# Kernel optimization log

Measured on AMD Instinct MI355X. Metric: run time of the kernel, lower is better.

The kernel has to match this reference:

```python
import jax, jax.numpy as jnp
import numpy as np

N = 50000   # nodes
E = 600000  # edges
D = 128     # node_features (EvolveGCNO in=out channels)
H = 128     # hidden_dim (final Linear out)


def setup_inputs() -> dict:
    key = jax.random.key(0)
    ks = jax.random.split(key, 9)
    stdv = 1.0 / np.sqrt(D)
    u = lambda k, shape: jax.random.uniform(k, shape, jnp.float32, -stdv, stdv)
    return {
        "x": jax.random.normal(ks[0], (N, D), jnp.float32),
        "edge_index": jax.random.randint(ks[1], (2, E), 0, N),
        "edge_weight": jax.random.uniform(ks[2], (E,), jnp.float32),
        "W0": u(ks[3], (D, D)),        # EvolveGCNO initial_weight (squeezed)
        "w_ih": u(ks[4], (3 * D, D)),  # GRU input weights (r|z|n)
        "w_hh": u(ks[5], (3 * D, D)),  # GRU hidden weights (r|z|n)
        "b_ih": u(ks[6], (3 * D,)),
        "b_hh": u(ks[7], (3 * D,)),
        "W_lin": u(ks[8], (H, D)),     # torch Linear weight [out, in]
        "b_lin": jnp.zeros((H,), jnp.float32),
    }


def _gru_step(x, h, w_ih, w_hh, b_ih, b_hh):
    # One torch.nn.GRU cell step; here x == h == W0 (weight evolution).
    gi = x @ w_ih.T + b_ih
    gh = h @ w_hh.T + b_hh
    i_r, i_z, i_n = jnp.split(gi, 3, axis=-1)
    h_r, h_z, h_n = jnp.split(gh, 3, axis=-1)
    r = jax.nn.sigmoid(i_r + h_r)
    z = jax.nn.sigmoid(i_z + h_z)
    n = jnp.tanh(i_n + r * h_n)
    return (1.0 - z) * n + z * h


def reference(x, edge_index, edge_weight, W0, w_ih, w_hh, b_ih, b_hh, W_lin, b_lin):
    # 1) Evolve the GCN weight with one GRU step (input = hidden = W0).
    W = _gru_step(W0, W0, w_ih, w_hh, b_ih, b_hh)  # [D, D]

    # 2) GCNConv_Fixed_W: add self-loops (weight 1), symmetric normalization.
    loops = jnp.arange(N)
    row = jnp.concatenate([edge_index[0], loops])  # source
    col = jnp.concatenate([edge_index[1], loops])  # target
    ew = jnp.concatenate([edge_weight, jnp.ones((N,), x.dtype)])
    deg = jax.ops.segment_sum(ew, col, num_segments=N)
    dinv = jnp.where(deg > 0, jax.lax.rsqrt(deg), 0.0)
    norm = dinv[row] * ew * dinv[col]  # [E+N]

    xw = x @ W                                        # [N, D]
    h = jax.ops.segment_sum(norm[:, None] * xw[row], col, num_segments=N)  # [N, D]

    # 3) ReLU + Linear
    h = jax.nn.relu(h)
    return h @ W_lin.T + b_lin  # [N, H]
```

## Files before the change

kernel.cpp:

```cpp
#include <hip/hip_runtime.h>
#include <hip/hip_bf16.h>

#define NN 50000
#define EE 600000
#define DD 128
#define CAP 48

typedef __attribute__((ext_vector_type(8))) __bf16 bf16x8;
typedef __attribute__((ext_vector_type(8))) short short8;
typedef __attribute__((ext_vector_type(4))) float f32x4;

__device__ __forceinline__ unsigned short f2bf(float f) {
    union { float f; unsigned u; } c; c.f = f;
    unsigned r = (c.u + 0x7fffu + ((c.u >> 16) & 1u)) >> 16;
    return (unsigned short)r;
}
__device__ __forceinline__ float bflo(unsigned u) {
    union { unsigned u; float f; } c; c.u = u << 16; return c.f;
}
__device__ __forceinline__ float bfhi(unsigned u) {
    union { unsigned u; float f; } c; c.u = u & 0xffff0000u; return c.f;
}

__global__ __launch_bounds__(256) void gru_kernel(
    const float* __restrict__ W0, const float* __restrict__ w_ih,
    const float* __restrict__ w_hh, const float* __restrict__ b_ih,
    const float* __restrict__ b_hh, unsigned short* __restrict__ Wbt)
{
    int idx = blockIdx.x * 256 + threadIdx.x;
    int i = idx >> 7, j = idx & 127;
    const float4* a  = (const float4*)(W0  + i * DD);
    const float4* pr = (const float4*)(w_ih + (j        ) * DD);
    const float4* pz = (const float4*)(w_ih + (j + 128  ) * DD);
    const float4* pn = (const float4*)(w_ih + (j + 256  ) * DD);
    const float4* qr = (const float4*)(w_hh + (j        ) * DD);
    const float4* qz = (const float4*)(w_hh + (j + 128  ) * DD);
    const float4* qn = (const float4*)(w_hh + (j + 256  ) * DD);
    float ir = 0.f, iz = 0.f, inn = 0.f, hr = 0.f, hz = 0.f, hn = 0.f;
    for (int d = 0; d < DD / 4; ++d) {
        float4 av = a[d];
        float4 t;
        t = pr[d]; ir  += av.x*t.x + av.y*t.y + av.z*t.z + av.w*t.w;
        t = pz[d]; iz  += av.x*t.x + av.y*t.y + av.z*t.z + av.w*t.w;
        t = pn[d]; inn += av.x*t.x + av.y*t.y + av.z*t.z + av.w*t.w;
        t = qr[d]; hr  += av.x*t.x + av.y*t.y + av.z*t.z + av.w*t.w;
        t = qz[d]; hz  += av.x*t.x + av.y*t.y + av.z*t.z + av.w*t.w;
        t = qn[d]; hn  += av.x*t.x + av.y*t.y + av.z*t.z + av.w*t.w;
    }
    ir += b_ih[j]; iz += b_ih[j + 128]; inn += b_ih[j + 256];
    hr += b_hh[j]; hz += b_hh[j + 128]; hn  += b_hh[j + 256];
    float r = 1.f / (1.f + expf(-(ir + hr)));
    float z = 1.f / (1.f + expf(-(iz + hz)));
    float n = tanhf(inn + r * hn);
    float w = (1.f - z) * n + z * W0[idx];
    Wbt[j * DD + i] = f2bf(w);
}

__global__ __launch_bounds__(256) void histfill_kernel(
    const int* __restrict__ row, const int* __restrict__ col,
    const float* __restrict__ ew,
    unsigned long long* __restrict__ cnt64, unsigned* __restrict__ edges)
{
    int e = blockIdx.x * 256 + threadIdx.x;
    if (e >= EE) return;
    int c = col[e];
    float w = ew[e];
    unsigned wfix = (unsigned)__float2uint_rn(w * 16777216.0f);
    unsigned long long pk = (1ULL << 32) | (unsigned long long)wfix;
    unsigned long long old = atomicAdd(&cnt64[c], pk);
    unsigned oldcnt = (unsigned)(old >> 32);
    unsigned wq = (unsigned)(w * 65536.0f);
    if (wq > 65535u) wq = 65535u;
    if (oldcnt < CAP)
        edges[(size_t)c * CAP + oldcnt] = (unsigned)row[e] | (wq << 16);
}

__global__ __launch_bounds__(256) void decode_kernel(
    const unsigned long long* __restrict__ cnt64,
    float* __restrict__ dinv, int* __restrict__ cnt)
{
    int i = blockIdx.x * 256 + threadIdx.x;
    if (i >= NN) return;
    unsigned long long p = cnt64[i];
    int n = (int)(p >> 32);
    cnt[i] = n < CAP ? n : CAP;
    float deg = 1.0f + (float)(unsigned)p * (1.0f / 16777216.0f);
    dinv[i] = rsqrtf(deg);
}

__global__ __launch_bounds__(256) void gather_kernel(
    const unsigned* __restrict__ edges, const int* __restrict__ cnt,
    const float* __restrict__ dinv,
    const unsigned* __restrict__ xwu, unsigned* __restrict__ hu)
{
    int wid  = threadIdx.x >> 6;
    int lane = threadIdx.x & 63;
    int node = blockIdx.x * 4 + wid;
    if (node >= NN) return;
    int n = cnt[node];
    const unsigned* eb = edges + (size_t)node * CAP;
    float ax = 0.f, ay = 0.f;
    int n4 = n & ~3;
    for (int k = 0; k < n4; k += 4) {
        uint4 rc = *(const uint4*)(eb + k);
        int s0 = (int)(rc.x & 0xFFFFu), s1 = (int)(rc.y & 0xFFFFu);
        int s2 = (int)(rc.z & 0xFFFFu), s3 = (int)(rc.w & 0xFFFFu);
        float v0 = (float)(rc.x >> 16) * (1.0f / 65536.0f) * dinv[s0];
        float v1 = (float)(rc.y >> 16) * (1.0f / 65536.0f) * dinv[s1];
        float v2 = (float)(rc.z >> 16) * (1.0f / 65536.0f) * dinv[s2];
        float v3 = (float)(rc.w >> 16) * (1.0f / 65536.0f) * dinv[s3];
        unsigned x0 = xwu[(size_t)s0 * 64 + lane];
        unsigned x1 = xwu[(size_t)s1 * 64 + lane];
        unsigned x2 = xwu[(size_t)s2 * 64 + lane];
        unsigned x3 = xwu[(size_t)s3 * 64 + lane];
        ax += v0 * bflo(x0) + v1 * bflo(x1) + v2 * bflo(x2) + v3 * bflo(x3);
        ay += v0 * bfhi(x0) + v1 * bfhi(x1) + v2 * bfhi(x2) + v3 * bfhi(x3);
    }
    for (int k = n4; k < n; ++k) {
        unsigned r0 = eb[k];
        int s0 = (int)(r0 & 0xFFFFu);
        float v0 = (float)(r0 >> 16) * (1.0f / 65536.0f) * dinv[s0];
        unsigned x0 = xwu[(size_t)s0 * 64 + lane];
        ax += v0 * bflo(x0); ay += v0 * bfhi(x0);
    }
    float s = dinv[node];
    hu[(size_t)node * 64 + lane] =
        (unsigned)f2bf(ax * s) | ((unsigned)f2bf(ay * s) << 16);
}

template <int MODE>
__global__ __launch_bounds__(256) void mfma_gemm(
    const float* __restrict__ Af, const short* __restrict__ hb,
    const short* __restrict__ xwb, const float* __restrict__ dinv,
    const short* __restrict__ Bb, const float* __restrict__ Bf,
    const float* __restrict__ bias,
    unsigned short* __restrict__ outb, float* __restrict__ outf)
{
    __shared__ __align__(16) short Bs[DD * DD];
    __shared__ __align__(16) short As[64 * DD];
    const int t = threadIdx.x;
    const int i0 = blockIdx.x * 64;

    if (MODE == 0) {
        for (int u = t; u < 2048; u += 256) {
            int byte = u << 4;
            int brow = byte >> 8;
            *(short8*)((char*)Bs + (byte ^ ((brow & 7) << 4))) =
                *(const short8*)((const char*)Bb + byte);
        }
    } else {
        for (int u = t; u < 2048; u += 256) {
            int brow = u >> 4;
            int kc = (u & 15) << 3;
            const float4* p = (const float4*)(Bf + brow * DD + kc);
            float4 f0 = p[0], f1 = p[1];
            short8 v;
            v[0] = (short)f2bf(f0.x); v[1] = (short)f2bf(f0.y);
            v[2] = (short)f2bf(f0.z); v[3] = (short)f2bf(f0.w);
            v[4] = (short)f2bf(f1.x); v[5] = (short)f2bf(f1.y);
            v[6] = (short)f2bf(f1.z); v[7] = (short)f2bf(f1.w);
            int byte = (brow << 8) + (kc << 1);
            *(short8*)((char*)Bs + (byte ^ ((brow & 7) << 4))) = v;
        }
    }

    for (int u = t; u < 1024; u += 256) {
        int arow = u >> 4;
        int kc = (u & 15) << 3;
        int grow = i0 + arow;
        short8 v;
#pragma unroll
        for (int i = 0; i < 8; ++i) v[i] = 0;
        if (grow < NN) {
            if (MODE == 0) {
                const float4* p = (const float4*)(Af + (size_t)grow * DD + kc);
                float4 f0 = p[0], f1 = p[1];
                v[0] = (short)f2bf(f0.x); v[1] = (short)f2bf(f0.y);
                v[2] = (short)f2bf(f0.z); v[3] = (short)f2bf(f0.w);
                v[4] = (short)f2bf(f1.x); v[5] = (short)f2bf(f1.y);
                v[6] = (short)f2bf(f1.z); v[7] = (short)f2bf(f1.w);
            } else {
                float s = dinv[grow]; s *= s;
                uint4 hu = *(const uint4*)(hb  + (size_t)grow * DD + kc);
                uint4 xu = *(const uint4*)(xwb + (size_t)grow * DD + kc);
                v[0] = (short)f2bf(fmaxf(bflo(hu.x) + s * bflo(xu.x), 0.f));
                v[1] = (short)f2bf(fmaxf(bfhi(hu.x) + s * bfhi(xu.x), 0.f));
                v[2] = (short)f2bf(fmaxf(bflo(hu.y) + s * bflo(xu.y), 0.f));
                v[3] = (short)f2bf(fmaxf(bfhi(hu.y) + s * bfhi(xu.y), 0.f));
                v[4] = (short)f2bf(fmaxf(bflo(hu.z) + s * bflo(xu.z), 0.f));
                v[5] = (short)f2bf(fmaxf(bfhi(hu.z) + s * bfhi(xu.z), 0.f));
                v[6] = (short)f2bf(fmaxf(bflo(hu.w) + s * bflo(xu.w), 0.f));
                v[7] = (short)f2bf(fmaxf(bfhi(hu.w) + s * bfhi(xu.w), 0.f));
            }
        }
        int byte = (arow << 8) + (kc << 1);
        *(short8*)((char*)As + (byte ^ ((arow & 7) << 4))) = v;
    }
    __syncthreads();

    const int lane = t & 63, wv = t >> 6;
    const int c0 = lane & 15, g = lane >> 4;
    const int arow = wv * 16 + c0;
    f32x4 acc[8];
#pragma unroll
    for (int n = 0; n < 8; ++n) { acc[n][0] = acc[n][1] = acc[n][2] = acc[n][3] = 0.f; }

#pragma unroll
    for (int s = 0; s < 4; ++s) {
        int k0 = s * 32 + g * 8;
        int abyte = (arow << 8) + (k0 << 1);
        bf16x8 a = *(const bf16x8*)((const char*)As + (abyte ^ ((arow & 7) << 4)));
#pragma unroll
        for (int n = 0; n < 8; ++n) {
            int bcol = n * 16 + c0;
            int bbyte = (bcol << 8) + (k0 << 1);
            bf16x8 b = *(const bf16x8*)((const char*)Bs + (bbyte ^ ((bcol & 7) << 4)));
            acc[n] = __builtin_amdgcn_mfma_f32_16x16x32_bf16(a, b, acc[n], 0, 0, 0);
        }
    }

#pragma unroll
    for (int n = 0; n < 8; ++n) {
        int ccol = n * 16 + c0;
        float bb = (MODE == 1) ? bias[ccol] : 0.f;
#pragma unroll
        for (int r = 0; r < 4; ++r) {
            int grow = i0 + wv * 16 + g * 4 + r;
            if (grow < NN) {
                if (MODE == 0)
                    outb[(size_t)grow * DD + ccol] = f2bf(acc[n][r]);
                else
                    outf[(size_t)grow * DD + ccol] = acc[n][r] + bb;
            }
        }
    }
}

extern "C" void kernel_launch(void* const* d_in, const int* in_sizes, int n_in,
                              void* d_out, int out_size, void* d_ws, size_t ws_size,
                              hipStream_t stream)
{
    const float* x    = (const float*)d_in[0];
    const int*   ei   = (const int*)d_in[1];
    const float* ew   = (const float*)d_in[2];
    const float* W0   = (const float*)d_in[3];
    const float* w_ih = (const float*)d_in[4];
    const float* w_hh = (const float*)d_in[5];
    const float* b_ih = (const float*)d_in[6];
    const float* b_hh = (const float*)d_in[7];
    const float* Wlin = (const float*)d_in[8];
    const float* blin = (const float*)d_in[9];
    float* out = (float*)d_out;

    const int* row = ei;
    const int* col = ei + EE;

    char* ws = (char*)d_ws;
    unsigned short* Wbt = (unsigned short*)ws;
    unsigned long long* cnt64 = (unsigned long long*)(ws + 32768);
    float* dinv = (float*)(ws + 435200);
    int*   cnt  = (int*)(ws + 635904);
    short* xw   = (short*)(ws + 836608);
    short* h    = (short*)(ws + 13636608);
    unsigned* edges = (unsigned*)(ws + 26436608);

    hipMemsetAsync(cnt64, 0, (size_t)NN * 8, stream);

    gru_kernel<<<64, 256, 0, stream>>>(W0, w_ih, w_hh, b_ih, b_hh, Wbt);

    histfill_kernel<<<(EE + 255) / 256, 256, 0, stream>>>(row, col, ew, cnt64, edges);

    decode_kernel<<<(NN + 255) / 256, 256, 0, stream>>>(cnt64, dinv, cnt);

    mfma_gemm<0><<<(NN + 63) / 64, 256, 0, stream>>>(
        x, nullptr, nullptr, nullptr, (const short*)Wbt, nullptr, nullptr,
        (unsigned short*)xw, nullptr);

    gather_kernel<<<(NN + 3) / 4, 256, 0, stream>>>(
        edges, cnt, dinv, (const unsigned*)xw, (unsigned*)h);

    mfma_gemm<1><<<(NN + 63) / 64, 256, 0, stream>>>(
        nullptr, h, xw, dinv, nullptr, Wlin, blin, nullptr, out);
}
```

Baseline: 140.5 us.

## Pack count and weight sum into 32-bit atomics and drop decode kernel

The 64-bit count/weight-sum atomic becomes a single 32-bit word: a 7-bit count sits above a 25-bit fixed-point weight sum at 16 fractional bits. The memset and the GRU kernel merge into one launch, and the decode kernel is removed. The gather and final GEMM now compute rsqrt(deg) on the fly from the packed word, and the gather loop is unrolled to 8 edges. This cuts two launches and the atomic width, but the degree precision becomes coarser and each gathered edge now recomputes an rsqrt.

```diff
diff --git a/kernel.cpp b/kernel.cpp
--- a/kernel.cpp
+++ b/kernel.cpp
@@ -5,6 +5,8 @@
 #define EE 600000
 #define DD 128
 #define CAP 48
+#define CNT_SHIFT 25
+#define SUM_MASK 0x1FFFFFFu
 
 typedef __attribute__((ext_vector_type(8))) __bf16 bf16x8;
 typedef __attribute__((ext_vector_type(8))) short short8;
@@ -21,13 +23,22 @@
 __device__ __forceinline__ float bfhi(unsigned u) {
     union { unsigned u; float f; } c; c.u = u & 0xffff0000u; return c.f;
 }
-
-__global__ __launch_bounds__(256) void gru_kernel(
+__device__ __forceinline__ float degof(unsigned p) {
+    return 1.0f + (float)(p & SUM_MASK) * (1.0f / 65536.0f);
+}
+
+__global__ __launch_bounds__(256) void init_gru_kernel(
+    unsigned* __restrict__ cnt32,
     const float* __restrict__ W0, const float* __restrict__ w_ih,
     const float* __restrict__ w_hh, const float* __restrict__ b_ih,
     const float* __restrict__ b_hh, unsigned short* __restrict__ Wbt)
 {
-    int idx = blockIdx.x * 256 + threadIdx.x;
+    if (blockIdx.x < 49) {
+        int i = blockIdx.x * 256 + threadIdx.x;
+        if (i < 50176 * 4 / 16) ((uint4*)cnt32)[i] = make_uint4(0u, 0u, 0u, 0u);
+        return;
+    }
+    int idx = (blockIdx.x - 49) * 256 + threadIdx.x;
     int i = idx >> 7, j = idx & 127;
     const float4* a  = (const float4*)(W0  + i * DD);
     const float4* pr = (const float4*)(w_ih + (j        ) * DD);
@@ -59,71 +70,89 @@
 __global__ __launch_bounds__(256) void histfill_kernel(
     const int* __restrict__ row, const int* __restrict__ col,
     const float* __restrict__ ew,
-    unsigned long long* __restrict__ cnt64, unsigned* __restrict__ edges)
+    unsigned* __restrict__ cnt32, unsigned* __restrict__ edges)
 {
     int e = blockIdx.x * 256 + threadIdx.x;
     if (e >= EE) return;
     int c = col[e];
-    float w = ew[e];
-    unsigned wfix = (unsigned)__float2uint_rn(w * 16777216.0f);
-    unsigned long long pk = (1ULL << 32) | (unsigned long long)wfix;
-    unsigned long long old = atomicAdd(&cnt64[c], pk);
-    unsigned oldcnt = (unsigned)(old >> 32);
-    unsigned wq = (unsigned)(w * 65536.0f);
+    unsigned wq = (unsigned)(ew[e] * 65536.0f);
     if (wq > 65535u) wq = 65535u;
+    unsigned old = atomicAdd(&cnt32[c], (1u << CNT_SHIFT) | wq);
+    unsigned oldcnt = old >> CNT_SHIFT;
     if (oldcnt < CAP)
         edges[(size_t)c * CAP + oldcnt] = (unsigned)row[e] | (wq << 16);
 }
 
-__global__ __launch_bounds__(256) void decode_kernel(
-    const unsigned long long* __restrict__ cnt64,
-    float* __restrict__ dinv, int* __restrict__ cnt)
-{
-    int i = blockIdx.x * 256 + threadIdx.x;
-    if (i >= NN) return;
-    unsigned long long p = cnt64[i];
-    int n = (int)(p >> 32);
-    cnt[i] = n < CAP ? n : CAP;
-    float deg = 1.0f + (float)(unsigned)p * (1.0f / 16777216.0f);
-    dinv[i] = rsqrtf(deg);
-}
-
 __global__ __launch_bounds__(256) void gather_kernel(
-    const unsigned* __restrict__ edges, const int* __restrict__ cnt,
-    const float* __restrict__ dinv,
+    const unsigned* __restrict__ edges, const unsigned* __restrict__ cnt32,
     const unsigned* __restrict__ xwu, unsigned* __restrict__ hu)
 {
     int wid  = threadIdx.x >> 6;
     int lane = threadIdx.x & 63;
     int node = blockIdx.x * 4 + wid;
     if (node >= NN) return;
-    int n = cnt[node];
+    unsigned pn = cnt32[node];
+    int n = (int)(pn >> CNT_SHIFT); if (n > CAP) n = CAP;
     const unsigned* eb = edges + (size_t)node * CAP;
     float ax = 0.f, ay = 0.f;
-    int n4 = n & ~3;
-    for (int k = 0; k < n4; k += 4) {
-        uint4 rc = *(const uint4*)(eb + k);
-        int s0 = (int)(rc.x & 0xFFFFu), s1 = (int)(rc.y & 0xFFFFu);
-        int s2 = (int)(rc.z & 0xFFFFu), s3 = (int)(rc.w & 0xFFFFu);
-        float v0 = (float)(rc.x >> 16) * (1.0f / 65536.0f) * dinv[s0];
-        float v1 = (float)(rc.y >> 16) * (1.0f / 65536.0f) * dinv[s1];
-        float v2 = (float)(rc.z >> 16) * (1.0f / 65536.0f) * dinv[s2];
-        float v3 = (float)(rc.w >> 16) * (1.0f / 65536.0f) * dinv[s3];
+    int k = 0;
+    int n8 = n & ~7;
+    for (; k < n8; k += 8) {
+        uint4 ra = *(const uint4*)(eb + k);
+        uint4 rb = *(const uint4*)(eb + k + 4);
+        int s0 = (int)(ra.x & 0xFFFFu), s1 = (int)(ra.y & 0xFFFFu);
+        int s2 = (int)(ra.z & 0xFFFFu), s3 = (int)(ra.w & 0xFFFFu);
+        int s4 = (int)(rb.x & 0xFFFFu), s5 = (int)(rb.y & 0xFFFFu);
+        int s6 = (int)(rb.z & 0xFFFFu), s7 = (int)(rb.w & 0xFFFFu);
+        unsigned p0 = cnt32[s0], p1 = cnt32[s1], p2 = cnt32[s2], p3 = cnt32[s3];
+        unsigned p4 = cnt32[s4], p5 = cnt32[s5], p6 = cnt32[s6], p7 = cnt32[s7];
         unsigned x0 = xwu[(size_t)s0 * 64 + lane];
         unsigned x1 = xwu[(size_t)s1 * 64 + lane];
         unsigned x2 = xwu[(size_t)s2 * 64 + lane];
         unsigned x3 = xwu[(size_t)s3 * 64 + lane];
+        unsigned x4 = xwu[(size_t)s4 * 64 + lane];
+        unsigned x5 = xwu[(size_t)s5 * 64 + lane];
+        unsigned x6 = xwu[(size_t)s6 * 64 + lane];
+        unsigned x7 = xwu[(size_t)s7 * 64 + lane];
+        float v0 = (float)(ra.x >> 16) * (1.0f / 65536.0f) * rsqrtf(degof(p0));
+        float v1 = (float)(ra.y >> 16) * (1.0f / 65536.0f) * rsqrtf(degof(p1));
+        float v2 = (float)(ra.z >> 16) * (1.0f / 65536.0f) * rsqrtf(degof(p2));
+        float v3 = (float)(ra.w >> 16) * (1.0f / 65536.0f) * rsqrtf(degof(p3));
+        float v4 = (float)(rb.x >> 16) * (1.0f / 65536.0f) * rsqrtf(degof(p4));
+        float v5 = (float)(rb.y >> 16) * (1.0f / 65536.0f) * rsqrtf(degof(p5));
+        float v6 = (float)(rb.z >> 16) * (1.0f / 65536.0f) * rsqrtf(degof(p6));
+        float v7 = (float)(rb.w >> 16) * (1.0f / 65536.0f) * rsqrtf(degof(p7));
+        ax += v0 * bflo(x0) + v1 * bflo(x1) + v2 * bflo(x2) + v3 * bflo(x3)
+            + v4 * bflo(x4) + v5 * bflo(x5) + v6 * bflo(x6) + v7 * bflo(x7);
+        ay += v0 * bfhi(x0) + v1 * bfhi(x1) + v2 * bfhi(x2) + v3 * bfhi(x3)
+            + v4 * bfhi(x4) + v5 * bfhi(x5) + v6 * bfhi(x6) + v7 * bfhi(x7);
+    }
+    int n4 = n & ~3;
+    for (; k < n4; k += 4) {
+        uint4 rc = *(const uint4*)(eb + k);
+        int s0 = (int)(rc.x & 0xFFFFu), s1 = (int)(rc.y & 0xFFFFu);
+        int s2 = (int)(rc.z & 0xFFFFu), s3 = (int)(rc.w & 0xFFFFu);
+        unsigned p0 = cnt32[s0], p1 = cnt32[s1], p2 = cnt32[s2], p3 = cnt32[s3];
+        unsigned x0 = xwu[(size_t)s0 * 64 + lane];
+        unsigned x1 = xwu[(size_t)s1 * 64 + lane];
+        unsigned x2 = xwu[(size_t)s2 * 64 + lane];
+        unsigned x3 = xwu[(size_t)s3 * 64 + lane];
+        float v0 = (float)(rc.x >> 16) * (1.0f / 65536.0f) * rsqrtf(degof(p0));
+        float v1 = (float)(rc.y >> 16) * (1.0f / 65536.0f) * rsqrtf(degof(p1));
+        float v2 = (float)(rc.z >> 16) * (1.0f / 65536.0f) * rsqrtf(degof(p2));
+        float v3 = (float)(rc.w >> 16) * (1.0f / 65536.0f) * rsqrtf(degof(p3));
         ax += v0 * bflo(x0) + v1 * bflo(x1) + v2 * bflo(x2) + v3 * bflo(x3);
         ay += v0 * bfhi(x0) + v1 * bfhi(x1) + v2 * bfhi(x2) + v3 * bfhi(x3);
     }
-    for (int k = n4; k < n; ++k) {
+    for (; k < n; ++k) {
         unsigned r0 = eb[k];
         int s0 = (int)(r0 & 0xFFFFu);
-        float v0 = (float)(r0 >> 16) * (1.0f / 65536.0f) * dinv[s0];
+        unsigned p0 = cnt32[s0];
         unsigned x0 = xwu[(size_t)s0 * 64 + lane];
+        float v0 = (float)(r0 >> 16) * (1.0f / 65536.0f) * rsqrtf(degof(p0));
         ax += v0 * bflo(x0); ay += v0 * bfhi(x0);
     }
-    float s = dinv[node];
+    float s = rsqrtf(degof(pn));
     hu[(size_t)node * 64 + lane] =
         (unsigned)f2bf(ax * s) | ((unsigned)f2bf(ay * s) << 16);
 }
@@ -131,7 +160,7 @@
 template <int MODE>
 __global__ __launch_bounds__(256) void mfma_gemm(
     const float* __restrict__ Af, const short* __restrict__ hb,
-    const short* __restrict__ xwb, const float* __restrict__ dinv,
+    const short* __restrict__ xwb, const unsigned* __restrict__ cnt32,
     const short* __restrict__ Bb, const float* __restrict__ Bf,
     const float* __restrict__ bias,
     unsigned short* __restrict__ outb, float* __restrict__ outf)
@@ -180,7 +209,7 @@
                 v[4] = (short)f2bf(f1.x); v[5] = (short)f2bf(f1.y);
                 v[6] = (short)f2bf(f1.z); v[7] = (short)f2bf(f1.w);
             } else {
-                float s = dinv[grow]; s *= s;
+                float s = 1.0f / degof(cnt32[grow]);
                 uint4 hu = *(const uint4*)(hb  + (size_t)grow * DD + kc);
                 uint4 xu = *(const uint4*)(xwb + (size_t)grow * DD + kc);
                 v[0] = (short)f2bf(fmaxf(bflo(hu.x) + s * bflo(xu.x), 0.f));
@@ -257,28 +286,22 @@
 
     char* ws = (char*)d_ws;
     unsigned short* Wbt = (unsigned short*)ws;
-    unsigned long long* cnt64 = (unsigned long long*)(ws + 32768);
-    float* dinv = (float*)(ws + 435200);
-    int*   cnt  = (int*)(ws + 635904);
-    short* xw   = (short*)(ws + 836608);
-    short* h    = (short*)(ws + 13636608);
-    unsigned* edges = (unsigned*)(ws + 26436608);
-
-    hipMemsetAsync(cnt64, 0, (size_t)NN * 8, stream);
-
-    gru_kernel<<<64, 256, 0, stream>>>(W0, w_ih, w_hh, b_ih, b_hh, Wbt);
-
-    histfill_kernel<<<(EE + 255) / 256, 256, 0, stream>>>(row, col, ew, cnt64, edges);
-
-    decode_kernel<<<(NN + 255) / 256, 256, 0, stream>>>(cnt64, dinv, cnt);
+    unsigned* cnt32 = (unsigned*)(ws + 32768);
+    short* xw   = (short*)(ws + 233472);
+    short* h    = (short*)(ws + 13033472);
+    unsigned* edges = (unsigned*)(ws + 25833472);
+
+    init_gru_kernel<<<113, 256, 0, stream>>>(cnt32, W0, w_ih, w_hh, b_ih, b_hh, Wbt);
+
+    histfill_kernel<<<(EE + 255) / 256, 256, 0, stream>>>(row, col, ew, cnt32, edges);
 
     mfma_gemm<0><<<(NN + 63) / 64, 256, 0, stream>>>(
         x, nullptr, nullptr, nullptr, (const short*)Wbt, nullptr, nullptr,
         (unsigned short*)xw, nullptr);
 
     gather_kernel<<<(NN + 3) / 4, 256, 0, stream>>>(
-        edges, cnt, dinv, (const unsigned*)xw, (unsigned*)h);
+        edges, cnt32, (const unsigned*)xw, (unsigned*)h);
 
     mfma_gemm<1><<<(NN + 63) / 64, 256, 0, stream>>>(
-        nullptr, h, xw, dinv, nullptr, Wlin, blin, nullptr, out);
-}
+        nullptr, h, xw, cnt32, nullptr, Wlin, blin, nullptr, out);
+}
```

New measurement: 131.0 us. 1.07x faster.
